# Performance work log

Hardware: AMD Instinct MI355X
Metric: run time of the kernel (lower is better)

Reference implementation:

```python
import jax, jax.numpy as jnp
from jax import lax
import numpy as np

HIDDEN = 128


def _gru_cell(x, h, W_ih, W_hh, b_ih, b_hh):
    # PyTorch GRUCell: gates ordered (r, z, n)
    gi = x @ W_ih.T + b_ih            # [B, 3H]
    gh = h @ W_hh.T + b_hh            # [B, 3H]
    i_r, i_z, i_n = jnp.split(gi, 3, axis=-1)
    h_r, h_z, h_n = jnp.split(gh, 3, axis=-1)
    r = jax.nn.sigmoid(i_r + h_r)
    z = jax.nn.sigmoid(i_z + h_z)
    n = jnp.tanh(i_n + r * h_n)
    return (1.0 - z) * n + z * h


def setup_inputs() -> dict:
    key = jax.random.key(0)
    ks = jax.random.split(key, 16)
    B, T, H = 4, 16384, HIDDEN
    f32 = jnp.float32
    rn = lambda k, s: jax.random.normal(k, s, dtype=f32)
    inp = {
        "pos_x": rn(ks[0], (B, T)),
        "pos_y": rn(ks[1], (B, T)),
        "v_x": rn(ks[2], (B, T)),
        "v_y": rn(ks[3], (B, T)),
        # embed: Linear(4, H)
        "W_embed": rn(ks[4], (H, 4)) * 0.05,
        "b_embed": jnp.zeros((H,), f32),
        # GRUCell(H, H)
        "W_ih": rn(ks[5], (3 * H, H)) * 0.05,
        "W_hh": rn(ks[6], (3 * H, H)) * 0.05,
        "b_ih": jnp.zeros((3 * H,), f32),
        "b_hh": jnp.zeros((3 * H,), f32),
        # fc head: H -> H/2 -> H/2 -> 2 with ELU
        "W1": rn(ks[7], (H // 2, H)) * 0.05,
        "b1": jnp.zeros((H // 2,), f32),
        "W2": rn(ks[8], (H // 2, H // 2)) * 0.05,
        "b2": jnp.zeros((H // 2,), f32),
        "W3": rn(ks[9], (2, H // 2)) * 0.05,
        "b3": jnp.zeros((2,), f32),
        # deterministic replacement for `epsilon > random.random()`:
        # 1 => feed hidden back as input after the context window
        "step_mask": jax.random.randint(ks[10], (T,), 0, 2).astype(jnp.int32),
        "context_frame_num": 8,
    }
    return inp


def reference(pos_x, pos_y, v_x, v_y, W_embed, b_embed, W_ih, W_hh, b_ih, b_hh,
              W1, b1, W2, b2, W3, b3, step_mask, context_frame_num):
    # stack -> [4, B, T] -> permute -> [B=4, T, feat=4]
    x = jnp.stack([pos_x, pos_y, v_x, v_y], axis=0).transpose(0, 2, 1)
    B, T = x.shape[0], x.shape[1]
    xe = x @ W_embed.T + b_embed                       # [B, T, H]

    idx = jnp.arange(T)
    # i == 0 always uses x (hidden is None); i < context uses x;
    # afterwards use x only when the sampled mask is 0.
    use_x = (idx < jnp.maximum(context_frame_num, 1)) | (step_mask == 0)

    def step(h, inputs):
        x_t, ux = inputs                               # x_t: [B, H]
        inp = jnp.where(ux, x_t, h)
        h_new = _gru_cell(inp, h, W_ih, W_hh, b_ih, b_hh)
        return h_new, h_new

    h0 = jnp.zeros((B, xe.shape[-1]), xe.dtype)
    _, hs = lax.scan(step, h0, (xe.transpose(1, 0, 2), use_x))  # hs: [T, B, H]

    # 3-layer MLP head applied to every step's hidden state (vectorized)
    y = jax.nn.elu(hs @ W1.T + b1)
    y = jax.nn.elu(y @ W2.T + b2)
    y = y @ W3.T + b3                                  # [T, B, 2]
    res = y.transpose(1, 0, 2)                         # [B, T, 2]
    return res[:, :, 0], res[:, :, 1]
```

## Files before the change

### kernel.cpp

```cpp
#include <hip/hip_runtime.h>
#include <hip/hip_fp16.h>

#define TLEN 16384
#define HD 128
#define L2E 1.4426950408889634f

typedef _Float16 v8h __attribute__((ext_vector_type(8)));
typedef float    v4f __attribute__((ext_vector_type(4)));

union U4H8 { uint4 u; v8h h; };

__device__ __forceinline__ v8h cvt8s(const float* p, float sc) {
    v8h r;
    #pragma unroll
    for (int i = 0; i < 8; ++i) r[i] = (_Float16)(p[i] * sc);
    return r;
}
__device__ __forceinline__ v8h cvt8sums(const float* p, const float* q, float sc) {
    v8h r;
    #pragma unroll
    for (int i = 0; i < 8; ++i) r[i] = (_Float16)((p[i] + q[i]) * sc);
    return r;
}
__device__ __forceinline__ unsigned int packh2(float a, float b) {
    union { _Float16 h[2]; unsigned int u; } c;
    c.h[0] = (_Float16)a; c.h[1] = (_Float16)b; return c.u;
}
__device__ __forceinline__ float selg(v4f a, int g) {
    const float lo = (g & 1) ? a.y : a.x;
    const float hi = (g & 1) ? a.w : a.z;
    return (g & 2) ? hi : lo;
}
__device__ __forceinline__ float fexp2(float x) {
    float r; asm("v_exp_f32 %0, %1" : "=v"(r) : "v"(x)); return r;
}
__device__ __forceinline__ float frcp(float x) {
    float r; asm("v_rcp_f32 %0, %1" : "=v"(r) : "v"(x)); return r;
}
#define PINA(x) asm volatile("" : "+a"(x))

#define BAR() asm volatile("s_waitcnt lgkmcnt(0)\n\ts_barrier" ::: "memory")

__device__ __forceinline__ v4f ch4(v8h a0, v8h a1, v8h a2, v8h a3,
                                   v8h B0, v8h B1, v8h B2, v8h B3, v4f c) {
    c = __builtin_amdgcn_mfma_f32_16x16x32_f16(a0, B0, c, 0, 0, 0);
    c = __builtin_amdgcn_mfma_f32_16x16x32_f16(a1, B1, c, 0, 0, 0);
    c = __builtin_amdgcn_mfma_f32_16x16x32_f16(a2, B2, c, 0, 0, 0);
    return __builtin_amdgcn_mfma_f32_16x16x32_f16(a3, B3, c, 0, 0, 0);
}
__device__ __forceinline__ float gru_h(float sRp, float sZp, float ginp,
                                       float ghnp, float hold) {
    const float r  = frcp(1.f + fexp2(sRp));
    const float z  = frcp(1.f + fexp2(sZp));
    const float e2 = fexp2(fmaf(r, ghnp, ginp));
    const float n  = fmaf(-2.f, frcp(e2 + 1.f), 1.f);
    return fmaf(z, hold - n, n);
}

__global__
__attribute__((amdgpu_flat_work_group_size(512, 512)))
void gru_kernel(
    const float* __restrict__ px,
    const float* __restrict__ py,
    const float* __restrict__ vx,
    const float* __restrict__ vy,
    const float* __restrict__ Wemb,
    const float* __restrict__ bemb,
    const float* __restrict__ Wih,
    const float* __restrict__ Whh,
    const float* __restrict__ bih,
    const float* __restrict__ bhh,
    const int*   __restrict__ step_mask,
    const int*   __restrict__ ctxp,
    unsigned short* __restrict__ hs)
{
    const int tid  = threadIdx.x;
    const int w    = tid >> 6;
    const int lane = tid & 63;
    const int m    = lane & 15;
    const int q8   = (lane >> 4) * 8;
    const int qq4  = (lane >> 4) * 4;
    const int cme  = lane & 3;
    const int gme  = (lane >> 2) & 3;
    const int kme  = 16 * w + qq4 + gme;

    __shared__ alignas(16) _Float16 h2L[2][4][176];
    __shared__ alignas(16) uint4 xpadL[256][4];
    __shared__ float WembL[512];
    __shared__ float bembL[128];
    __shared__ alignas(16) float Wc4[384][4];
    __shared__ float bfoldL[384];

    v8h ahr0, ahr1, ahr2, ahr3, ahz0, ahz1, ahz2, ahz3, ahn0, ahn1, ahn2, ahn3;
    v8h ain0, ain1, ain2, ain3;
    v8h asr0, asr1, asr2, asr3, asz0, asz1, asz2, asz3;
    {
        const float sRZ = -L2E, sN = 2.f * L2E;
        const float* pr = Whh + (size_t)(      16 * w + m) * 128 + q8;
        const float* pz = Whh + (size_t)(128 + 16 * w + m) * 128 + q8;
        const float* pn = Whh + (size_t)(256 + 16 * w + m) * 128 + q8;
        const float* qr = Wih + (size_t)(      16 * w + m) * 128 + q8;
        const float* qz = Wih + (size_t)(128 + 16 * w + m) * 128 + q8;
        const float* qn = Wih + (size_t)(256 + 16 * w + m) * 128 + q8;
        ahr0 = cvt8s(pr, sRZ); ahr1 = cvt8s(pr + 32, sRZ); ahr2 = cvt8s(pr + 64, sRZ); ahr3 = cvt8s(pr + 96, sRZ);
        ahz0 = cvt8s(pz, sRZ); ahz1 = cvt8s(pz + 32, sRZ); ahz2 = cvt8s(pz + 64, sRZ); ahz3 = cvt8s(pz + 96, sRZ);
        ahn0 = cvt8s(pn, sN);  ahn1 = cvt8s(pn + 32, sN);  ahn2 = cvt8s(pn + 64, sN);  ahn3 = cvt8s(pn + 96, sN);
        ain0 = cvt8s(qn, sN);  ain1 = cvt8s(qn + 32, sN);  ain2 = cvt8s(qn + 64, sN);  ain3 = cvt8s(qn + 96, sN);
        asr0 = cvt8sums(pr, qr, sRZ);           asr1 = cvt8sums(pr + 32, qr + 32, sRZ);
        asr2 = cvt8sums(pr + 64, qr + 64, sRZ); asr3 = cvt8sums(pr + 96, qr + 96, sRZ);
        asz0 = cvt8sums(pz, qz, sRZ);           asz1 = cvt8sums(pz + 32, qz + 32, sRZ);
        asz2 = cvt8sums(pz + 64, qz + 64, sRZ); asz3 = cvt8sums(pz + 96, qz + 96, sRZ);
    }
    PINA(ahr0); PINA(ahr1); PINA(ahr2); PINA(ahr3);
    PINA(ahz0); PINA(ahz1); PINA(ahz2); PINA(ahz3);
    PINA(ahn0); PINA(ahn1); PINA(ahn2); PINA(ahn3);
    PINA(ain0); PINA(ain1); PINA(ain2); PINA(ain3);
    PINA(asr0); PINA(asr1); PINA(asr2); PINA(asr3);
    PINA(asz0); PINA(asz1); PINA(asz2); PINA(asz3);

    const int rB = 16 * w + qq4;
    v4f bSR, bSZ, bHN, bIN;
    #pragma unroll
    for (int j = 0; j < 4; ++j) {
        bSR[j] = -L2E * (bih[rB + j]       + bhh[rB + j]);
        bSZ[j] = -L2E * (bih[128 + rB + j] + bhh[128 + rB + j]);
        bHN[j] = 2.f * L2E * bhh[256 + rB + j];
        bIN[j] = 2.f * L2E * bih[256 + rB + j];
    }

    WembL[tid] = Wemb[tid];
    if (tid < 128) bembL[tid] = bemb[tid];
    for (int i = tid; i < 2 * 4 * 176; i += 512) ((_Float16*)h2L)[i] = (_Float16)0.f;
    __syncthreads();
    if (tid < 384) {
        const float* wr = Wih + (size_t)tid * 128;
        float c0 = 0.f, c1 = 0.f, c2 = 0.f, c3 = 0.f, cb = 0.f;
        #pragma unroll 4
        for (int j = 0; j < 128; ++j) {
            const float wv = wr[j];
            const float4 e = *(const float4*)&WembL[j * 4];
            c0 = fmaf(wv, e.x, c0); c1 = fmaf(wv, e.y, c1);
            c2 = fmaf(wv, e.z, c2); c3 = fmaf(wv, e.w, c3);
            cb = fmaf(wv, bembL[j], cb);
        }
        Wc4[tid][0] = c0; Wc4[tid][1] = c1; Wc4[tid][2] = c2; Wc4[tid][3] = c3;
        bfoldL[tid] = cb;
    }
    __syncthreads();
    v8h wcr = {}, wcz = {}, wcn = {};
    if (lane < 16) {
        const int r0 = 16 * w + m, r1 = 128 + r0, r2 = 256 + r0;
        wcr[0] = (_Float16)(-L2E * Wc4[r0][0]); wcr[1] = (_Float16)(-L2E * Wc4[r0][1]);
        wcr[2] = (_Float16)(-L2E * Wc4[r0][2]); wcr[3] = (_Float16)(-L2E * Wc4[r0][3]);
        wcr[4] = (_Float16)(-L2E * bfoldL[r0]);
        wcz[0] = (_Float16)(-L2E * Wc4[r1][0]); wcz[1] = (_Float16)(-L2E * Wc4[r1][1]);
        wcz[2] = (_Float16)(-L2E * Wc4[r1][2]); wcz[3] = (_Float16)(-L2E * Wc4[r1][3]);
        wcz[4] = (_Float16)(-L2E * bfoldL[r1]);
        wcn[0] = (_Float16)(2.f * L2E * Wc4[r2][0]); wcn[1] = (_Float16)(2.f * L2E * Wc4[r2][1]);
        wcn[2] = (_Float16)(2.f * L2E * Wc4[r2][2]); wcn[3] = (_Float16)(2.f * L2E * Wc4[r2][3]);
        wcn[4] = (_Float16)(2.f * L2E * bfoldL[r2]);
    }
    PINA(wcr); PINA(wcz); PINA(wcn);

    const int ctxm = (ctxp[0] < 1) ? 1 : ctxp[0];
    float hold1 = 0.f;

    const uint4* rdA = (const uint4*)&h2L[0][cme][0] + (lane >> 4);
    const uint4* rdB = (const uint4*)&h2L[1][cme][0] + (lane >> 4);
    _Float16*    wrA = &h2L[1][cme][kme];
    _Float16*    wrB = &h2L[0][cme][kme];
    unsigned short* hp = hs + (size_t)cme * (TLEN * 128) + kme;

#define STEP(RD, WR, XOFF, HOFF, UX)                                         \
    {                                                                        \
        U4H8 b0, b1, b2, b3;                                                 \
        b0.u = (RD)[0]; b1.u = (RD)[4]; b2.u = (RD)[8]; b3.u = (RD)[12];     \
        v4f aR, aZ, aNi;                                                     \
        v4f aNh = ch4(ahn0, ahn1, ahn2, ahn3, b0.h, b1.h, b2.h, b3.h, bHN);  \
        if (!(UX)) {                                                         \
            aR  = ch4(asr0, asr1, asr2, asr3, b0.h, b1.h, b2.h, b3.h, bSR);  \
            aNi = ch4(ain0, ain1, ain2, ain3, b0.h, b1.h, b2.h, b3.h, bIN);  \
            aZ  = ch4(asz0, asz1, asz2, asz3, b0.h, b1.h, b2.h, b3.h, bSZ);  \
        } else {                                                             \
            U4H8 xb; xb.u = xq[XOFF];                                        \
            aR  = ch4(ahr0, ahr1, ahr2, ahr3, b0.h, b1.h, b2.h, b3.h, bSR);  \
            aR  = __builtin_amdgcn_mfma_f32_16x16x32_f16(wcr, xb.h, aR, 0, 0, 0); \
            aNi = __builtin_amdgcn_mfma_f32_16x16x32_f16(wcn, xb.h, bIN, 0, 0, 0); \
            aZ  = ch4(ahz0, ahz1, ahz2, ahz3, b0.h, b1.h, b2.h, b3.h, bSZ);  \
            aZ  = __builtin_amdgcn_mfma_f32_16x16x32_f16(wcz, xb.h, aZ, 0, 0, 0); \
        }                                                                    \
        const float hnew = gru_h(selg(aR, gme), selg(aZ, gme),               \
                                 selg(aNi, gme), selg(aNh, gme), hold1);     \
        hold1 = hnew;                                                        \
        union { _Float16 f; unsigned short u; } hv; hv.f = (_Float16)hnew;   \
        *(WR) = hv.f;                                                        \
        hp[HOFF] = hv.u;                                                     \
        BAR();                                                               \
    }

    for (int t0 = 0; t0 < TLEN; t0 += 256) {
        for (int i = tid; i < 1024; i += 512) {
            const int t = i >> 2, c = i & 3;
            const int gt = t0 + t;
            const float* xa = (c == 0) ? px : (c == 1) ? py : (c == 2) ? vx : vy;
            uint4 u;
            u.x = packh2(xa[gt],            xa[TLEN + gt]);
            u.y = packh2(xa[2 * TLEN + gt], xa[3 * TLEN + gt]);
            u.z = packh2(1.f, 0.f);
            u.w = 0u;
            xpadL[t][c] = u;
        }
        unsigned long long mb0, mb1, mb2, mb3;
        {
            const int tb = t0 + lane;
            mb0 = __ballot((tb       < ctxm) || (step_mask[tb      ] == 0));
            mb1 = __ballot((tb +  64 < ctxm) || (step_mask[tb +  64] == 0));
            mb2 = __ballot((tb + 128 < ctxm) || (step_mask[tb + 128] == 0));
            mb3 = __ballot((tb + 192 < ctxm) || (step_mask[tb + 192] == 0));
        }
        BAR();
        const uint4* xq = (const uint4*)&xpadL[0][cme];
        #pragma unroll 1
        for (int j = 0; j < 4; ++j) {
            const unsigned long long mj =
                (j == 0) ? mb0 : (j == 1) ? mb1 : (j == 2) ? mb2 : mb3;
            #pragma unroll 1
            for (int t2 = 0; t2 < 64; t2 += 8) {
                const unsigned u0 = (unsigned)(mj >> t2);
                STEP(rdA, wrA,  0,   0, (u0      ) & 1u);
                STEP(rdB, wrB,  4, 128, (u0 >> 1) & 1u);
                STEP(rdA, wrA,  8, 256, (u0 >> 2) & 1u);
                STEP(rdB, wrB, 12, 384, (u0 >> 3) & 1u);
                STEP(rdA, wrA, 16, 512, (u0 >> 4) & 1u);
                STEP(rdB, wrB, 20, 640, (u0 >> 5) & 1u);
                STEP(rdA, wrA, 24, 768, (u0 >> 6) & 1u);
                STEP(rdB, wrB, 28, 896, (u0 >> 7) & 1u);
                xq += 32;
                hp += 1024;
            }
        }
    }
#undef STEP
}

__global__ __launch_bounds__(64) void head_kernel(
    const float*  __restrict__ W1,
    const float*  __restrict__ b1,
    const float*  __restrict__ W2,
    const float*  __restrict__ b2,
    const float*  __restrict__ W3,
    const float*  __restrict__ b3,
    const __half* __restrict__ hs,
    float*        __restrict__ out)
{
    __shared__ float W1L[64 * 128];
    __shared__ float W2L[64 * 64];
    __shared__ float W3L[2 * 64];
    __shared__ float b1L[64], b2L[64], b3L[2];
    __shared__ float y1L[64 * 65];

    const int tid = threadIdx.x;
    {
        float4* dst1 = (float4*)W1L; const float4* src1 = (const float4*)W1;
        for (int i = tid; i < 2048; i += 64) dst1[i] = src1[i];
        float4* dst2 = (float4*)W2L; const float4* src2 = (const float4*)W2;
        for (int i = tid; i < 1024; i += 64) dst2[i] = src2[i];
        if (tid < 32) ((float4*)W3L)[tid] = ((const float4*)W3)[tid];
        b1L[tid] = b1[tid];
        b2L[tid] = b2[tid];
        if (tid < 2) b3L[tid] = b3[tid];
    }
    __syncthreads();

    const int row = blockIdx.x * 64 + tid;
    float h[128];
    {
        const uint4* hp = (const uint4*)(hs + (size_t)row * HD);
        #pragma unroll
        for (int c = 0; c < 16; ++c) {
            uint4 q = hp[c];
            const __half2* hh = (const __half2*)&q;
            #pragma unroll
            for (int d = 0; d < 4; ++d) {
                const float2 f = __half22float2(hh[d]);
                h[c*8 + d*2 + 0] = f.x;
                h[c*8 + d*2 + 1] = f.y;
            }
        }
    }
    for (int l = 0; l < 64; ++l) {
        float a0 = b1L[l], a1 = 0.f;
        #pragma unroll
        for (int j = 0; j < 128; j += 4) {
            const float4 wv = *(const float4*)&W1L[l*128 + j];
            a0 = fmaf(wv.x, h[j+0], a0);
            a1 = fmaf(wv.y, h[j+1], a1);
            a0 = fmaf(wv.z, h[j+2], a0);
            a1 = fmaf(wv.w, h[j+3], a1);
        }
        const float acc = a0 + a1;
        y1L[tid * 65 + l] = (acc > 0.f) ? acc : (__expf(acc) - 1.f);
    }
    float y30 = b3L[0], y31 = b3L[1];
    for (int l = 0; l < 64; ++l) {
        float a0 = b2L[l], a1 = 0.f;
        const int yb = tid * 65;
        #pragma unroll
        for (int j = 0; j < 64; j += 4) {
            const float4 wv = *(const float4*)&W2L[l*64 + j];
            a0 = fmaf(wv.x, y1L[yb + j+0], a0);
            a1 = fmaf(wv.y, y1L[yb + j+1], a1);
            a0 = fmaf(wv.z, y1L[yb + j+2], a0);
            a1 = fmaf(wv.w, y1L[yb + j+3], a1);
        }
        const float acc = a0 + a1;
        const float v = (acc > 0.f) ? acc : (__expf(acc) - 1.f);
        y30 = fmaf(W3L[l],      v, y30);
        y31 = fmaf(W3L[64 + l], v, y31);
    }
    out[row]            = y30;
    out[4 * TLEN + row] = y31;
}

extern "C" void kernel_launch(void* const* d_in, const int* in_sizes, int n_in,
                              void* d_out, int out_size, void* d_ws, size_t ws_size,
                              hipStream_t stream) {
    const float* px   = (const float*)d_in[0];
    const float* py   = (const float*)d_in[1];
    const float* vx   = (const float*)d_in[2];
    const float* vy   = (const float*)d_in[3];
    const float* Wemb = (const float*)d_in[4];
    const float* bemb = (const float*)d_in[5];
    const float* Wih  = (const float*)d_in[6];
    const float* Whh  = (const float*)d_in[7];
    const float* bih  = (const float*)d_in[8];
    const float* bhh  = (const float*)d_in[9];
    const float* W1   = (const float*)d_in[10];
    const float* b1   = (const float*)d_in[11];
    const float* W2   = (const float*)d_in[12];
    const float* b2   = (const float*)d_in[13];
    const float* W3   = (const float*)d_in[14];
    const float* b3   = (const float*)d_in[15];
    const int* step_mask = (const int*)d_in[16];
    const int* ctx       = (const int*)d_in[17];
    unsigned short* hs = (unsigned short*)d_ws;
    float* out = (float*)d_out;

    hipLaunchKernelGGL(gru_kernel, dim3(1), dim3(512), 0, stream,
                       px, py, vx, vy, Wemb, bemb, Wih, Whh, bih, bhh,
                       step_mask, ctx, hs);
    hipLaunchKernelGGL(head_kernel, dim3(1024), dim3(64), 0, stream,
                       W1, b1, W2, b2, W3, b3, (const __half*)hs, out);
}
```

Baseline: 7.109 ms.

## Double-buffer input chunk staging and prefetch next chunk during recurrence

The per-256-step input staging and mask ballots are moved off the critical path. The next chunk's global loads are issued before the recurrence loop, then written into a second LDS buffer after the first 64 steps, so the old per-chunk barrier and its exposed global-load latency go away. It also moves the aNh MFMA into each branch so it can be scheduled alongside the other gate products. The cost is extra LDS and live registers for the prefetched values, which adds register pressure in a kernel that already pins many register-resident weights.

```diff
diff --git a/kernel.cpp b/kernel.cpp
--- a/kernel.cpp
+++ b/kernel.cpp
@@ -84,8 +84,12 @@
     const int gme  = (lane >> 2) & 3;
     const int kme  = 16 * w + qq4 + gme;
 
+    const int pc = tid & 3;
+    const int pt = tid >> 2;
+    const float* pxa = (pc == 0) ? px : (pc == 1) ? py : (pc == 2) ? vx : vy;
+
     __shared__ alignas(16) _Float16 h2L[2][4][176];
-    __shared__ alignas(16) uint4 xpadL[256][4];
+    __shared__ alignas(16) uint4 xpadL[2][256][4];
     __shared__ float WembL[512];
     __shared__ float bembL[128];
     __shared__ alignas(16) float Wc4[384][4];
@@ -128,9 +132,26 @@
         bIN[j] = 2.f * L2E * bih[256 + rB + j];
     }
 
+    const int ctxm = (ctxp[0] < 1) ? 1 : ctxp[0];
+
     WembL[tid] = Wemb[tid];
     if (tid < 128) bembL[tid] = bemb[tid];
     for (int i = tid; i < 2 * 4 * 176; i += 512) ((_Float16*)h2L)[i] = (_Float16)0.f;
+    unsigned long long mb0, mb1, mb2, mb3;
+    {
+        uint4 u;
+        u.z = packh2(1.f, 0.f); u.w = 0u;
+        u.x = packh2(pxa[pt],            pxa[TLEN + pt]);
+        u.y = packh2(pxa[2 * TLEN + pt], pxa[3 * TLEN + pt]);
+        xpadL[0][pt][pc] = u;
+        u.x = packh2(pxa[128 + pt],            pxa[TLEN + 128 + pt]);
+        u.y = packh2(pxa[2 * TLEN + 128 + pt], pxa[3 * TLEN + 128 + pt]);
+        xpadL[0][pt + 128][pc] = u;
+        mb0 = __ballot((lane       < ctxm) || (step_mask[lane      ] == 0));
+        mb1 = __ballot((lane +  64 < ctxm) || (step_mask[lane +  64] == 0));
+        mb2 = __ballot((lane + 128 < ctxm) || (step_mask[lane + 128] == 0));
+        mb3 = __ballot((lane + 192 < ctxm) || (step_mask[lane + 192] == 0));
+    }
     __syncthreads();
     if (tid < 384) {
         const float* wr = Wih + (size_t)tid * 128;
@@ -162,7 +183,6 @@
     }
     PINA(wcr); PINA(wcz); PINA(wcn);
 
-    const int ctxm = (ctxp[0] < 1) ? 1 : ctxp[0];
     float hold1 = 0.f;
 
     const uint4* rdA = (const uint4*)&h2L[0][cme][0] + (lane >> 4);
@@ -175,16 +195,17 @@
     {                                                                        \
         U4H8 b0, b1, b2, b3;                                                 \
         b0.u = (RD)[0]; b1.u = (RD)[4]; b2.u = (RD)[8]; b3.u = (RD)[12];     \
-        v4f aR, aZ, aNi;                                                     \
-        v4f aNh = ch4(ahn0, ahn1, ahn2, ahn3, b0.h, b1.h, b2.h, b3.h, bHN);  \
+        v4f aR, aZ, aNh, aNi;                                                \
         if (!(UX)) {                                                         \
             aR  = ch4(asr0, asr1, asr2, asr3, b0.h, b1.h, b2.h, b3.h, bSR);  \
+            aNh = ch4(ahn0, ahn1, ahn2, ahn3, b0.h, b1.h, b2.h, b3.h, bHN);  \
             aNi = ch4(ain0, ain1, ain2, ain3, b0.h, b1.h, b2.h, b3.h, bIN);  \
             aZ  = ch4(asz0, asz1, asz2, asz3, b0.h, b1.h, b2.h, b3.h, bSZ);  \
         } else {                                                             \
             U4H8 xb; xb.u = xq[XOFF];                                        \
             aR  = ch4(ahr0, ahr1, ahr2, ahr3, b0.h, b1.h, b2.h, b3.h, bSR);  \
             aR  = __builtin_amdgcn_mfma_f32_16x16x32_f16(wcr, xb.h, aR, 0, 0, 0); \
+            aNh = ch4(ahn0, ahn1, ahn2, ahn3, b0.h, b1.h, b2.h, b3.h, bHN);  \
             aNi = __builtin_amdgcn_mfma_f32_16x16x32_f16(wcn, xb.h, bIN, 0, 0, 0); \
             aZ  = ch4(ahz0, ahz1, ahz2, ahz3, b0.h, b1.h, b2.h, b3.h, bSZ);  \
             aZ  = __builtin_amdgcn_mfma_f32_16x16x32_f16(wcz, xb.h, aZ, 0, 0, 0); \
@@ -198,28 +219,26 @@
         BAR();                                                               \
     }
 
+    int cur = 0;
     for (int t0 = 0; t0 < TLEN; t0 += 256) {
-        for (int i = tid; i < 1024; i += 512) {
-            const int t = i >> 2, c = i & 3;
-            const int gt = t0 + t;
-            const float* xa = (c == 0) ? px : (c == 1) ? py : (c == 2) ? vx : vy;
-            uint4 u;
-            u.x = packh2(xa[gt],            xa[TLEN + gt]);
-            u.y = packh2(xa[2 * TLEN + gt], xa[3 * TLEN + gt]);
-            u.z = packh2(1.f, 0.f);
-            u.w = 0u;
-            xpadL[t][c] = u;
-        }
-        unsigned long long mb0, mb1, mb2, mb3;
-        {
-            const int tb = t0 + lane;
-            mb0 = __ballot((tb       < ctxm) || (step_mask[tb      ] == 0));
-            mb1 = __ballot((tb +  64 < ctxm) || (step_mask[tb +  64] == 0));
-            mb2 = __ballot((tb + 128 < ctxm) || (step_mask[tb + 128] == 0));
-            mb3 = __ballot((tb + 192 < ctxm) || (step_mask[tb + 192] == 0));
-        }
-        BAR();
-        const uint4* xq = (const uint4*)&xpadL[0][cme];
+        const int  t0n  = t0 + 256;
+        const bool more = (t0n < TLEN);
+        const int  nxt  = cur ^ 1;
+        float f0 = 0.f, f1 = 0.f, f2 = 0.f, f3 = 0.f;
+        float f4 = 0.f, f5 = 0.f, f6 = 0.f, f7 = 0.f;
+        int   n0 = 0, n1 = 0, n2 = 0, n3 = 0;
+        if (more) {
+            const int g = t0n + pt;
+            f0 = pxa[g];                  f1 = pxa[TLEN + g];
+            f2 = pxa[2 * TLEN + g];       f3 = pxa[3 * TLEN + g];
+            f4 = pxa[128 + g];            f5 = pxa[TLEN + 128 + g];
+            f6 = pxa[2 * TLEN + 128 + g]; f7 = pxa[3 * TLEN + 128 + g];
+            const int tb = t0n + lane;
+            n0 = step_mask[tb];       n1 = step_mask[tb + 64];
+            n2 = step_mask[tb + 128]; n3 = step_mask[tb + 192];
+        }
+        const uint4* xq = (const uint4*)&xpadL[cur][0][cme];
+        unsigned long long nmb0 = 0, nmb1 = 0, nmb2 = 0, nmb3 = 0;
         #pragma unroll 1
         for (int j = 0; j < 4; ++j) {
             const unsigned long long mj =
@@ -238,7 +257,21 @@
                 xq += 32;
                 hp += 1024;
             }
-        }
+            if (j == 0 && more) {
+                uint4 u;
+                u.z = packh2(1.f, 0.f); u.w = 0u;
+                u.x = packh2(f0, f1);   u.y = packh2(f2, f3);
+                xpadL[nxt][pt][pc] = u;
+                u.x = packh2(f4, f5);   u.y = packh2(f6, f7);
+                xpadL[nxt][pt + 128][pc] = u;
+                const int tb = t0n + lane;
+                nmb0 = __ballot((tb       < ctxm) || (n0 == 0));
+                nmb1 = __ballot((tb +  64 < ctxm) || (n1 == 0));
+                nmb2 = __ballot((tb + 128 < ctxm) || (n2 == 0));
+                nmb3 = __ballot((tb + 192 < ctxm) || (n3 == 0));
+            }
+        }
+        if (more) { mb0 = nmb0; mb1 = nmb1; mb2 = nmb2; mb3 = nmb3; cur = nxt; }
     }
 #undef STEP
 }
```

After: 7.732 ms. 1.09x slower.
